# Kernel optimization log

Measured on AMD Instinct MI355X. Metric: run time of the kernel, lower is better.

Reference implementation:

```python
import jax, jax.numpy as jnp
import numpy as np

D = 1024
H = 16
FF = 4 * D


def layer_norm(x, g, b, eps=1e-5):
    mu = jnp.mean(x, axis=-1, keepdims=True)
    var = jnp.var(x, axis=-1, keepdims=True)
    return (x - mu) * jax.lax.rsqrt(var + eps) * g + b


def setup_inputs() -> dict:
    key = jax.random.key(0)
    ks = jax.random.split(key, 8)
    s = lambda fan_in: 1.0 / np.sqrt(fan_in)
    return {
        "x": jax.random.normal(ks[0], (2, 2048, D), dtype=jnp.float32),
        "ln1_g": jnp.ones((D,), jnp.float32),
        "ln1_b": jnp.zeros((D,), jnp.float32),
        "w_qkv": jax.random.uniform(ks[1], (D, 3 * D), jnp.float32, -s(D), s(D)),
        "b_qkv": jnp.zeros((3 * D,), jnp.float32),
        "w_out": jax.random.uniform(ks[2], (D, D), jnp.float32, -s(D), s(D)),
        "b_out": jnp.zeros((D,), jnp.float32),
        "ln2_g": jnp.ones((D,), jnp.float32),
        "ln2_b": jnp.zeros((D,), jnp.float32),
        "w_fc1": jax.random.uniform(ks[3], (D, FF), jnp.float32, -s(D), s(D)),
        "b_fc1": jnp.zeros((FF,), jnp.float32),
        "w_fc2": jax.random.uniform(ks[4], (FF, D), jnp.float32, -s(FF), s(FF)),
        "b_fc2": jnp.zeros((D,), jnp.float32),
    }


def reference(x, ln1_g, ln1_b, w_qkv, b_qkv, w_out, b_out,
              ln2_g, ln2_b, w_fc1, b_fc1, w_fc2, b_fc2):
    b, n, c = x.shape
    hd = c // H
    scale = hd ** -0.5

    # --- pre-norm MHA ---
    h = layer_norm(x, ln1_g, ln1_b)
    qkv = h @ w_qkv + b_qkv                      # [b,n,3c]
    qkv = qkv.reshape(b, n, 3, H, hd)
    q = jnp.transpose(qkv[:, :, 0], (0, 2, 1, 3))  # [b,H,n,hd]
    k = jnp.transpose(qkv[:, :, 1], (0, 2, 1, 3))
    v = jnp.transpose(qkv[:, :, 2], (0, 2, 1, 3))
    attn = jnp.einsum('bhqd,bhkd->bhqk', q, k) * scale
    attn = jax.nn.softmax(attn, axis=-1)
    o = jnp.einsum('bhqk,bhkd->bhqd', attn, v)   # [b,H,n,hd]
    o = jnp.transpose(o, (0, 2, 1, 3)).reshape(b, n, c)
    x = x + (o @ w_out + b_out)

    # --- pre-norm FFN ---
    h = layer_norm(x, ln2_g, ln2_b)
    h = jax.nn.gelu(h @ w_fc1 + b_fc1, approximate=False)
    x = x + (h @ w_fc2 + b_fc2)
    return x
```

## Files before the change

kernel.cpp:

```cpp
#include <hip/hip_runtime.h>
#include <stdint.h>
#include <math.h>

#define D_MODEL 1024
#define NHEAD   16
#define HDIM    64
#define FFDIM   4096
#define SEQ     2048
#define BATCH   2
#define NTOK    (BATCH*SEQ)
#define QKVN    (3*D_MODEL)

typedef __bf16 bf16;
typedef __attribute__((ext_vector_type(8))) __bf16 bf16x8;
typedef __attribute__((ext_vector_type(4))) __bf16 bf16x4;
typedef __attribute__((ext_vector_type(4))) float f32x4;

__device__ __forceinline__ void gld_lds16(const void* g, void* l) {
    __builtin_amdgcn_global_load_lds((__attribute__((address_space(1))) void*)g,
                                     (__attribute__((address_space(3))) void*)l,
                                     16, 0, 0);
}

__device__ __forceinline__ float fast_exp2(float x) {
#if __has_builtin(__builtin_amdgcn_exp2f)
    return __builtin_amdgcn_exp2f(x);
#else
    return __expf(x * 0.69314718056f);
#endif
}

__device__ __forceinline__ float fast_rcp(float x) {
#if __has_builtin(__builtin_amdgcn_rcpf)
    return __builtin_amdgcn_rcpf(x);
#else
    return 1.0f / x;
#endif
}

__device__ __forceinline__ float gelu_fast(float x) {
    float xx = x * x;
    float y  = x * fmaf(0.035677408137f, xx, 0.7978845608f);
    float z  = fminf(-2.8853900817779268f * y, 126.0f);
    float e  = fast_exp2(z);
    return x * fast_rcp(1.0f + e);
}

#define SYNC_VM(N) do {                                        \
    asm volatile("s_waitcnt vmcnt(" #N ")" ::: "memory");      \
    __builtin_amdgcn_s_barrier();                              \
    asm volatile("" ::: "memory");                             \
} while (0)

#define PHASE_BAR() do {                                       \
    asm volatile("s_waitcnt vmcnt(0)" ::: "memory");           \
    __builtin_amdgcn_s_barrier();                              \
    asm volatile("" ::: "memory");                             \
} while (0)

#define GEMM_BAR() do {                                        \
    asm volatile("s_waitcnt lgkmcnt(0)" ::: "memory");         \
    __builtin_amdgcn_s_barrier();                              \
    asm volatile("" ::: "memory");                             \
} while (0)

__global__ __launch_bounds__(256)
void k_transpose_all(const float* __restrict__ w_qkv, const float* __restrict__ w_out,
                     const float* __restrict__ w_fc1, const float* __restrict__ w_fc2,
                     bf16* __restrict__ t_qkv, bf16* __restrict__ t_out,
                     bf16* __restrict__ t_fc1, bf16* __restrict__ t_fc2) {
    __shared__ float tile[32][33];
    int bid = blockIdx.x;
    const float* W; bf16* Wt; int K, N, ti;
    if (bid < 3072)       { W = w_qkv; Wt = t_qkv; K = 1024; N = 3072; ti = bid; }
    else if (bid < 4096)  { W = w_out; Wt = t_out; K = 1024; N = 1024; ti = bid - 3072; }
    else if (bid < 8192)  { W = w_fc1; Wt = t_fc1; K = 1024; N = 4096; ti = bid - 4096; }
    else                  { W = w_fc2; Wt = t_fc2; K = 4096; N = 1024; ti = bid - 8192; }
    int tn = N >> 5;
    int n0 = (ti % tn) * 32, k0 = (ti / tn) * 32;
    int tx = threadIdx.x, ty = threadIdx.y;
#pragma unroll
    for (int i = 0; i < 4; i++)
        tile[ty + i * 8][tx] = W[(size_t)(k0 + ty + i * 8) * N + n0 + tx];
    __syncthreads();
#pragma unroll
    for (int i = 0; i < 4; i++)
        Wt[(size_t)(n0 + ty + i * 8) * K + k0 + tx] = (bf16)tile[tx][ty + i * 8];
}

__global__ __launch_bounds__(256)
void k_vtrans(const bf16* __restrict__ qkv, bf16* __restrict__ vT) {
    __shared__ bf16 t[32][33];
    int tok0 = blockIdx.x * 32, f0 = blockIdx.y * 32;
    int tx = threadIdx.x, ty = threadIdx.y;
#pragma unroll
    for (int i = 0; i < 4; i++)
        t[ty + i * 8][tx] = qkv[(size_t)(tok0 + ty + i * 8) * QKVN + 2 * D_MODEL + f0 + tx];
    __syncthreads();
    int s = tx;
    int pp = (s < 16) ? ((s >> 2) * 8 + (s & 3))
                      : (((s - 16) >> 2) * 8 + ((s - 16) & 3) + 4);
#pragma unroll
    for (int i = 0; i < 4; i++)
        vT[(size_t)(f0 + ty + i * 8) * NTOK + tok0 + pp] = t[tx][ty + i * 8];
}

__global__ __launch_bounds__(256)
void k_layernorm(const float* __restrict__ x, const float* __restrict__ g,
                 const float* __restrict__ b, bf16* __restrict__ out) {
    int row = blockIdx.x;
    int tid = threadIdx.x;
    float4 v = ((const float4*)(x + (size_t)row * D_MODEL))[tid];
    float s  = v.x + v.y + v.z + v.w;
    float ss = v.x * v.x + v.y * v.y + v.z * v.z + v.w * v.w;
#pragma unroll
    for (int off = 32; off > 0; off >>= 1) {
        s  += __shfl_down(s, off, 64);
        ss += __shfl_down(ss, off, 64);
    }
    __shared__ float red[2][4];
    __shared__ float mv[2];
    int wave = tid >> 6, lane = tid & 63;
    if (lane == 0) { red[0][wave] = s; red[1][wave] = ss; }
    __syncthreads();
    if (tid == 0) {
        float S  = red[0][0] + red[0][1] + red[0][2] + red[0][3];
        float SS = red[1][0] + red[1][1] + red[1][2] + red[1][3];
        float mu = S * (1.0f / D_MODEL);
        float var = SS * (1.0f / D_MODEL) - mu * mu;
        mv[0] = mu;
        mv[1] = rsqrtf(var + 1e-5f);
    }
    __syncthreads();
    float mu = mv[0], rs = mv[1];
    float4 gv = ((const float4*)g)[tid];
    float4 bv = ((const float4*)b)[tid];
    bf16x4 ov = { (bf16)((v.x - mu) * rs * gv.x + bv.x),
                  (bf16)((v.y - mu) * rs * gv.y + bv.y),
                  (bf16)((v.z - mu) * rs * gv.z + bv.z),
                  (bf16)((v.w - mu) * rs * gv.w + bv.w) };
    *(bf16x4*)(out + (size_t)row * D_MODEL + tid * 4) = ov;
}

template <int DO_GELU>
__global__ __launch_bounds__(512, 2)
void k_gemm256(const bf16* __restrict__ A, const bf16* __restrict__ Bt,
               const float* __restrict__ bias, bf16* __restrict__ outb,
               int M, int N, int K) {
    __shared__ bf16 LA[2][2][8192];
    __shared__ bf16 LB[2][2][8192];

    int tid = threadIdx.x;
    int wid = tid >> 6, lane = tid & 63;
    int quad = lane >> 4, l16 = lane & 15;
    int wm = (wid >> 2) * 128;
    int wn = (wid & 3) * 64;

    int nwg = gridDim.x * gridDim.y;
    int bid = blockIdx.y * gridDim.x + blockIdx.x;
    int sid = (bid & 7) * (nwg >> 3) + (bid >> 3);
    int bx = sid % gridDim.x, by = sid / gridDim.x;
    int m0 = by * 256, n0 = bx * 256;

    int l = lane;
    int rsw = l >> 2;
    int csw = 8 * ((l & 3) ^ ((l >> 3) & 3));
    const bf16* pA = A  + (size_t)(m0 + 32 * wid + rsw) * K + csw;
    const bf16* pB = Bt + (size_t)(n0 + 32 * wid + rsw) * K + csw;
    int sbase = wid * 1024;

    int xq = 8 * (quad ^ ((l16 >> 1) & 3));

    f32x4 acc[8][4];
#pragma unroll
    for (int i = 0; i < 8; i++)
#pragma unroll
        for (int j = 0; j < 4; j++) acc[i][j] = (f32x4){0.f, 0.f, 0.f, 0.f};

#define STAGE_A(buf, kh, t) do {                                               \
    gld_lds16(pA + (size_t)(t) * 64 + (kh) * 32,              &LA[buf][kh][sbase]);       \
    gld_lds16(pA + (size_t)16 * K + (size_t)(t) * 64 + (kh) * 32, &LA[buf][kh][sbase + 512]); \
} while (0)
#define STAGE_B(buf, kh, t) do {                                               \
    gld_lds16(pB + (size_t)(t) * 64 + (kh) * 32,              &LB[buf][kh][sbase]);       \
    gld_lds16(pB + (size_t)16 * K + (size_t)(t) * 64 + (kh) * 32, &LB[buf][kh][sbase + 512]); \
} while (0)

    bf16x8 af[4], bfr[4];
#define RD_B(buf, kh)  do {                                                    \
    _Pragma("unroll")                                                          \
    for (int fc = 0; fc < 4; fc++)                                             \
        bfr[fc] = *(const bf16x8*)&LB[buf][kh][(wn + fc * 16 + l16) * 32 + xq];\
} while (0)
#define RD_A(buf, kh, rh) do {                                                 \
    _Pragma("unroll")                                                          \
    for (int fr = 0; fr < 4; fr++)                                             \
        af[fr] = *(const bf16x8*)&LA[buf][kh][(wm + (rh) * 64 + fr * 16 + l16) * 32 + xq]; \
} while (0)
#define MFMA16(rh) do {                                                        \
    __builtin_amdgcn_s_setprio(1);                                             \
    _Pragma("unroll")                                                          \
    for (int fr = 0; fr < 4; fr++)                                             \
        _Pragma("unroll")                                                      \
        for (int fc = 0; fc < 4; fc++)                                         \
            acc[(rh) * 4 + fr][fc] =                                           \
                __builtin_amdgcn_mfma_f32_16x16x32_bf16(af[fr], bfr[fc],       \
                                                        acc[(rh) * 4 + fr][fc], 0, 0, 0); \
    __builtin_amdgcn_s_setprio(0);                                             \
} while (0)

    int nt = K / 64;
    int buf = 0;
    STAGE_A(0, 0, 0); STAGE_B(0, 0, 0); STAGE_A(0, 1, 0); STAGE_B(0, 1, 0);

    for (int t = 0; t < nt - 1; t++) {
        SYNC_VM(4);
        STAGE_A(buf ^ 1, 0, t + 1);
        RD_B(buf, 0); RD_A(buf, 0, 0);
        STAGE_B(buf ^ 1, 0, t + 1);
        MFMA16(0);
        RD_A(buf, 0, 1);
        MFMA16(1);
        SYNC_VM(4);
        STAGE_A(buf ^ 1, 1, t + 1);
        RD_B(buf, 1); RD_A(buf, 1, 0);
        STAGE_B(buf ^ 1, 1, t + 1);
        MFMA16(0);
        RD_A(buf, 1, 1);
        MFMA16(1);
        buf ^= 1;
    }
    SYNC_VM(4);
    RD_B(buf, 0); RD_A(buf, 0, 0);
    MFMA16(0);
    RD_A(buf, 0, 1);
    MFMA16(1);
    SYNC_VM(0);
    RD_B(buf, 1); RD_A(buf, 1, 0);
    MFMA16(0);
    RD_A(buf, 1, 1);
    MFMA16(1);

#undef STAGE_A
#undef STAGE_B
#undef RD_A
#undef RD_B
#undef MFMA16

#pragma unroll
    for (int fi = 0; fi < 8; fi++) {
        int row = m0 + wm + fi * 16 + quad * 4;
#pragma unroll
        for (int fc = 0; fc < 4; fc++) {
            int col = n0 + wn + fc * 16 + l16;
            float bb = bias[col];
#pragma unroll
            for (int r = 0; r < 4; r++) {
                float v = acc[fi][fc][r] + bb;
                if (DO_GELU) v = gelu_fast(v);
                outb[(size_t)(row + r) * N + col] = (bf16)v;
            }
        }
    }
}

template <int DO_GELU, int DO_RES, int OUT_BF16, int BN, int PIPE2, int SPLITK, int STAGE>
__global__ __launch_bounds__(256)
void k_gemm(const bf16* __restrict__ A, const bf16* __restrict__ Bt,
            const float* __restrict__ bias, const float* __restrict__ res,
            float* __restrict__ outf, bf16* __restrict__ outb,
            int M, int N, int K) {
    constexpr int WN = BN / 32;
    __shared__ bf16 As[2][128 * 32];
    __shared__ bf16 Bs[2][BN * 32];
    int tid  = threadIdx.x;
    int wave = tid >> 6, lane = tid & 63;
    int quad = lane >> 4, l16 = lane & 15;

    int nwg = gridDim.x * gridDim.y;
    int bid = blockIdx.y * gridDim.x + blockIdx.x;
    int sid = (bid & 7) * (nwg >> 3) + (bid >> 3);
    int bx = sid % gridDim.x, by = sid / gridDim.x;
    int m0 = by * 128, n0 = bx * BN;
    int wm = (wave >> 1) * 64, wn = (wave & 1) * (BN / 2);

    int Keff = (SPLITK == 2) ? (K >> 1) : K;
    int koff = (SPLITK == 2) ? blockIdx.z * Keff : 0;

    f32x4 acc[4][WN];
#pragma unroll
    for (int i = 0; i < 4; i++)
#pragma unroll
        for (int j = 0; j < WN; j++) acc[i][j] = (f32x4){0.f, 0.f, 0.f, 0.f};

    int lrow = lane >> 2;
    int lcol = (lane & 3) * 8;
    const bf16* gA0 = A + (size_t)(m0 + wave * 32 + lrow) * K + koff + lcol;
    const bf16* gA1 = gA0 + (size_t)16 * K;
    const bf16* gB0;
    const bf16* gB1 = nullptr;
    if constexpr (BN == 128) {
        gB0 = Bt + (size_t)(n0 + wave * 32 + lrow) * K + koff + lcol;
        gB1 = gB0 + (size_t)16 * K;
    } else {
        gB0 = Bt + (size_t)(n0 + wave * 16 + lrow) * K + koff + lcol;
    }

    int wA0 = wave * 1024 + lane * 8;
    int wA1 = wA0 + 512;
    int wB0 = (BN == 128) ? (wave * 1024 + lane * 8) : (wave * 512 + lane * 8);
    int wB1 = wB0 + 512;

    auto issue = [&](bf16x8* r, int k0) {
        r[0] = *(const bf16x8*)(gA0 + k0);
        r[1] = *(const bf16x8*)(gA1 + k0);
        r[2] = *(const bf16x8*)(gB0 + k0);
        if constexpr (BN == 128) r[3] = *(const bf16x8*)(gB1 + k0);
    };
    auto commit = [&](int buf, const bf16x8* r) {
        *(bf16x8*)(&As[buf][wA0]) = r[0];
        *(bf16x8*)(&As[buf][wA1]) = r[1];
        *(bf16x8*)(&Bs[buf][wB0]) = r[2];
        if constexpr (BN == 128) *(bf16x8*)(&Bs[buf][wB1]) = r[3];
    };
    auto compute = [&](const bf16* cA, const bf16* cB) {
        bf16x8 af[4], bfr[WN];
#pragma unroll
        for (int mi = 0; mi < 4; mi++)
            af[mi] = *(const bf16x8*)(cA + (wm + mi * 16 + l16) * 32 + quad * 8);
#pragma unroll
        for (int ni = 0; ni < WN; ni++)
            bfr[ni] = *(const bf16x8*)(cB + (wn + ni * 16 + l16) * 32 + quad * 8);
#pragma unroll
        for (int mi = 0; mi < 4; mi++)
#pragma unroll
            for (int ni = 0; ni < WN; ni++)
                acc[mi][ni] = __builtin_amdgcn_mfma_f32_16x16x32_bf16(af[mi], bfr[ni], acc[mi][ni], 0, 0, 0);
    };

    int niter = Keff / 32;
    if constexpr (STAGE == 1) {
        bf16* sA  = &As[0][wave * 1024];
        bf16* sB  = &Bs[0][(BN == 128) ? wave * 1024 : wave * 512];
        bf16* sA2 = &As[1][wave * 1024];
        bf16* sB2 = &Bs[1][(BN == 128) ? wave * 1024 : wave * 512];
        const bf16* rA  = &As[0][0]; const bf16* rB  = &Bs[0][0];
        const bf16* rA2 = &As[1][0]; const bf16* rB2 = &Bs[1][0];
        gld_lds16(gA0, sA);
        gld_lds16(gA1, sA + 512);
        gld_lds16(gB0, sB);
        if constexpr (BN == 128) gld_lds16(gB1, sB + 512);
        PHASE_BAR();
        for (int t = 1; t < niter; t++) {
            int k0 = t * 32;
            gld_lds16(gA0 + k0, sA2);
            gld_lds16(gA1 + k0, sA2 + 512);
            gld_lds16(gB0 + k0, sB2);
            if constexpr (BN == 128) gld_lds16(gB1 + k0, sB2 + 512);
            compute(rA, rB);
            PHASE_BAR();
            bf16* t0 = sA; sA = sA2; sA2 = t0;
            bf16* t1 = sB; sB = sB2; sB2 = t1;
            const bf16* t2 = rA; rA = rA2; rA2 = t2;
            const bf16* t3 = rB; rB = rB2; rB2 = t3;
        }
        compute(rA, rB);
    } else if constexpr (!PIPE2) {
        bf16x8 r0[4];
        issue(r0, 0);
        commit(0, r0);
        __syncthreads();
        for (int t = 1; t < niter; t++) {
            issue(r0, t * 32);
            compute(&As[(t - 1) & 1][0], &Bs[(t - 1) & 1][0]);
            commit(t & 1, r0);
            __syncthreads();
        }
        compute(&As[(niter - 1) & 1][0], &Bs[(niter - 1) & 1][0]);
    } else {
        bf16x8 r0[4], r1[4];
        issue(r0, 0);
        commit(0, r0);
        issue(r1, 32);
        GEMM_BAR();
        for (int t = 1; t + 2 < niter; t += 2) {
            issue(r0, (t + 1) * 32);
            compute(&As[0][0], &Bs[0][0]);
            commit(1, r1);
            GEMM_BAR();
            issue(r1, (t + 2) * 32);
            compute(&As[1][0], &Bs[1][0]);
            commit(0, r0);
            GEMM_BAR();
        }
        compute(&As[0][0], &Bs[0][0]);
        commit(1, r1);
        GEMM_BAR();
        compute(&As[1][0], &Bs[1][0]);
    }

#pragma unroll
    for (int mi = 0; mi < 4; mi++) {
        int row = m0 + wm + mi * 16 + quad * 4;
#pragma unroll
        for (int ni = 0; ni < WN; ni++) {
            int col = n0 + wn + ni * 16 + l16;
            if constexpr (SPLITK == 2) {
                float bb = (blockIdx.z == 0) ? bias[col] : 0.0f;
#pragma unroll
                for (int r = 0; r < 4; r++)
                    atomicAdd(&outf[(size_t)(row + r) * N + col], acc[mi][ni][r] + bb);
                continue;
            }
            float bb = bias[col];
#pragma unroll
            for (int r = 0; r < 4; r++) {
                float v = acc[mi][ni][r] + bb;
                if (DO_GELU) v = gelu_fast(v);
                size_t idx = (size_t)(row + r) * N + col;
                if (DO_RES) v += res[idx];
                if (OUT_BF16) outb[idx] = (bf16)v;
                else          outf[idx] = v;
            }
        }
    }
}

__global__ __launch_bounds__(256)
void k_attention2(const bf16* __restrict__ qkv, const bf16* __restrict__ vT,
                  bf16* __restrict__ o) {
    __shared__ bf16 Ks[2][2][64][32];
    __shared__ bf16 Vs[2][2][64][32];

    int tid = threadIdx.x, wave = tid >> 6, lane = tid & 63;
    int quad = lane >> 4, l16 = lane & 15;
    int bh = blockIdx.y;
    int b = bh >> 4, h = bh & 15;
    int q0 = blockIdx.x * 64 + wave * 16;

    const bf16* Qb  = qkv + (size_t)b * SEQ * QKVN + h * HDIM;
    const bf16* Kb  = Qb + D_MODEL;
    const bf16* vTb = vT + (size_t)h * HDIM * NTOK + b * SEQ;

    const float QSCALE = 0.125f * 1.44269504089f;
    bf16x8 qf[2];
#pragma unroll
    for (int c = 0; c < 2; c++) {
        bf16x8 qraw = *(const bf16x8*)(Qb + (size_t)(q0 + l16) * QKVN + c * 32 + quad * 8);
#pragma unroll
        for (int i = 0; i < 8; i++) qf[c][i] = (bf16)((float)qraw[i] * QSCALE);
    }

    const bf16* gK0 = Kb + (size_t)(wave * 16 + (lane >> 2)) * QKVN + (lane & 3) * 8;
    const bf16* gK1 = gK0 + 32;
    const bf16* gV0 = vTb + (size_t)(wave * 16 + (lane >> 2)) * NTOK + (lane & 3) * 8;
    const bf16* gV1 = gV0 + 32;

    f32x4 oacc[4];
#pragma unroll
    for (int i = 0; i < 4; i++) oacc[i] = (f32x4){0.f, 0.f, 0.f, 0.f};
    float lsum = 0.f;

    gld_lds16(gK0, &Ks[0][0][wave * 16][0]);
    gld_lds16(gK1, &Ks[0][1][wave * 16][0]);
    gld_lds16(gV0, &Vs[0][0][wave * 16][0]);
    gld_lds16(gV1, &Vs[0][1][wave * 16][0]);
    PHASE_BAR();

    int buf = 0;
    for (int kv0 = 0; kv0 < SEQ; kv0 += 64) {
        if (kv0 + 64 < SEQ) {
            size_t koff = (size_t)(kv0 + 64) * QKVN;
            gld_lds16(gK0 + koff, &Ks[buf ^ 1][0][wave * 16][0]);
            gld_lds16(gK1 + koff, &Ks[buf ^ 1][1][wave * 16][0]);
            gld_lds16(gV0 + kv0 + 64, &Vs[buf ^ 1][0][wave * 16][0]);
            gld_lds16(gV1 + kv0 + 64, &Vs[buf ^ 1][1][wave * 16][0]);
        }

        f32x4 s[4];
#pragma unroll
        for (int t = 0; t < 4; t++) {
            bf16x8 af0 = *(const bf16x8*)(&Ks[buf][0][t * 16 + l16][quad * 8]);
            bf16x8 af1 = *(const bf16x8*)(&Ks[buf][1][t * 16 + l16][quad * 8]);
            f32x4 z = (f32x4){0.f, 0.f, 0.f, 0.f};
            z = __builtin_amdgcn_mfma_f32_16x16x32_bf16(af0, qf[0], z, 0, 0, 0);
            z = __builtin_amdgcn_mfma_f32_16x16x32_bf16(af1, qf[1], z, 0, 0, 0);
            s[t] = z;
        }

        bf16x4 p[4];
#pragma unroll
        for (int t = 0; t < 4; t++)
#pragma unroll
            for (int r = 0; r < 4; r++) {
                float pf = fast_exp2(s[t][r]);
                lsum += pf;
                p[t][r] = (bf16)pf;
            }

#pragma unroll
        for (int tp = 0; tp < 2; tp++) {
            bf16x8 pa = __builtin_shufflevector(p[2 * tp], p[2 * tp + 1], 0, 1, 2, 3, 4, 5, 6, 7);
#pragma unroll
            for (int nt = 0; nt < 4; nt++) {
                bf16x8 vb = *(const bf16x8*)(&Vs[buf][tp][nt * 16 + l16][quad * 8]);
                oacc[nt] = __builtin_amdgcn_mfma_f32_16x16x32_bf16(pa, vb, oacc[nt], 0, 0, 0);
            }
        }

        PHASE_BAR();
        buf ^= 1;
    }

    lsum += __shfl_xor(lsum, 16, 64);
    lsum += __shfl_xor(lsum, 32, 64);
    float invl[4];
#pragma unroll
    for (int r = 0; r < 4; r++)
        invl[r] = 1.0f / __shfl(lsum, quad * 4 + r, 16);

#pragma unroll
    for (int nt = 0; nt < 4; nt++)
#pragma unroll
        for (int r = 0; r < 4; r++)
            o[(size_t)(b * SEQ + q0 + quad * 4 + r) * D_MODEL + h * HDIM + nt * 16 + l16] =
                (bf16)(oacc[nt][r] * invl[r]);
}

extern "C" void kernel_launch(void* const* d_in, const int* in_sizes, int n_in,
                              void* d_out, int out_size, void* d_ws, size_t ws_size,
                              hipStream_t stream) {
    const float* x     = (const float*)d_in[0];
    const float* ln1_g = (const float*)d_in[1];
    const float* ln1_b = (const float*)d_in[2];
    const float* w_qkv = (const float*)d_in[3];
    const float* b_qkv = (const float*)d_in[4];
    const float* w_out = (const float*)d_in[5];
    const float* b_out = (const float*)d_in[6];
    const float* ln2_g = (const float*)d_in[7];
    const float* ln2_b = (const float*)d_in[8];
    const float* w_fc1 = (const float*)d_in[9];
    const float* b_fc1 = (const float*)d_in[10];
    const float* w_fc2 = (const float*)d_in[11];
    const float* b_fc2 = (const float*)d_in[12];
    float* out = (float*)d_out;

    uintptr_t ws = (uintptr_t)d_ws;
    bf16* wt_qkv = (bf16*)(ws + 0);
    bf16* wt_out = (bf16*)(ws + 6291456);
    bf16* wt_fc1 = (bf16*)(ws + 8388608);
    bf16* wt_fc2 = (bf16*)(ws + 16777216);
    bf16* hbuf   = (bf16*)(ws + 25165824);
    bf16* vT     = hbuf;
    bf16* qkv    = (bf16*)(ws + 33554432);
    bf16* attn_o = (bf16*)(ws + 58720256);
    bf16* hgelu  = (bf16*)(ws + 33554432);

    k_transpose_all<<<12288, dim3(32, 8), 0, stream>>>(w_qkv, w_out, w_fc1, w_fc2,
                                                       wt_qkv, wt_out, wt_fc1, wt_fc2);

    k_layernorm<<<NTOK, 256, 0, stream>>>(x, ln1_g, ln1_b, hbuf);

    k_gemm256<0><<<dim3(QKVN / 256, NTOK / 256), 512, 0, stream>>>(
        hbuf, wt_qkv, b_qkv, qkv, NTOK, QKVN, D_MODEL);

    k_vtrans<<<dim3(NTOK / 32, D_MODEL / 32), dim3(32, 8), 0, stream>>>(qkv, vT);

    k_attention2<<<dim3(SEQ / 64, BATCH * NHEAD), 256, 0, stream>>>(qkv, vT, attn_o);

    k_gemm<0, 1, 0, 64, 1, 1, 0><<<dim3(D_MODEL / 64, NTOK / 128), 256, 0, stream>>>(
        attn_o, wt_out, b_out, x, out, nullptr, NTOK, D_MODEL, D_MODEL);

    k_layernorm<<<NTOK, 256, 0, stream>>>(out, ln2_g, ln2_b, hbuf);

    k_gemm256<1><<<dim3(FFDIM / 256, NTOK / 256), 512, 0, stream>>>(
        hbuf, wt_fc1, b_fc1, hgelu, NTOK, FFDIM, D_MODEL);

    k_gemm<0, 0, 0, 128, 1, 2, 0><<<dim3(D_MODEL / 128, NTOK / 128, 2), 256, 0, stream>>>(
        hgelu, wt_fc2, b_fc2, nullptr, out, nullptr, NTOK, D_MODEL, FFDIM);
}
```

Baseline: 353.3 us.

## Run FC2 on 256x256 split-K GEMM and rework k_gemm256 barrier schedule

Extends the 256x256 tile GEMM with split-K and atomic fp32 accumulation, and uses it for the FC2 projection (split into 4 along K) in place of the 128x128 split-K-by-2 kernel. It also reorders the k_gemm256 main loop so LDS reads are issued before the next global-to-LDS stage, with explicit barriers and lgkmcnt waits around each MFMA block. Unused k_gemm pipeline variants are removed. The aim is more reuse per loaded tile and better overlap in FC2, at the cost of more atomic traffic and extra barriers per k-step.

```diff
diff --git a/kernel.cpp b/kernel.cpp
--- a/kernel.cpp
+++ b/kernel.cpp
@@ -46,11 +46,12 @@
     return x * fast_rcp(1.0f + e);
 }
 
-#define SYNC_VM(N) do {                                        \
-    asm volatile("s_waitcnt vmcnt(" #N ")" ::: "memory");      \
+#define BARRIER() do {                                         \
     __builtin_amdgcn_s_barrier();                              \
     asm volatile("" ::: "memory");                             \
 } while (0)
+#define LGKM0() asm volatile("s_waitcnt lgkmcnt(0)" ::: "memory")
+#define VMW(N)  asm volatile("s_waitcnt vmcnt(" #N ")" ::: "memory")
 
 #define PHASE_BAR() do {                                       \
     asm volatile("s_waitcnt vmcnt(0)" ::: "memory");           \
@@ -142,11 +143,11 @@
     *(bf16x4*)(out + (size_t)row * D_MODEL + tid * 4) = ov;
 }
 
-template <int DO_GELU>
+template <int DO_GELU, int ATOMIC, int SPLITK>
 __global__ __launch_bounds__(512, 2)
 void k_gemm256(const bf16* __restrict__ A, const bf16* __restrict__ Bt,
                const float* __restrict__ bias, bf16* __restrict__ outb,
-               int M, int N, int K) {
+               float* __restrict__ outf, int M, int N, int K) {
     __shared__ bf16 LA[2][2][8192];
     __shared__ bf16 LB[2][2][8192];
 
@@ -162,11 +163,14 @@
     int bx = sid % gridDim.x, by = sid / gridDim.x;
     int m0 = by * 256, n0 = bx * 256;
 
+    int Keff = (SPLITK > 1) ? (K / SPLITK) : K;
+    int koff = (SPLITK > 1) ? blockIdx.z * Keff : 0;
+
     int l = lane;
     int rsw = l >> 2;
     int csw = 8 * ((l & 3) ^ ((l >> 3) & 3));
-    const bf16* pA = A  + (size_t)(m0 + 32 * wid + rsw) * K + csw;
-    const bf16* pB = Bt + (size_t)(n0 + 32 * wid + rsw) * K + csw;
+    const bf16* pA = A  + (size_t)(m0 + 32 * wid + rsw) * K + koff + csw;
+    const bf16* pB = Bt + (size_t)(n0 + 32 * wid + rsw) * K + koff + csw;
     int sbase = wid * 1024;
 
     int xq = 8 * (quad ^ ((l16 >> 1) & 3));
@@ -209,36 +213,49 @@
     __builtin_amdgcn_s_setprio(0);                                             \
 } while (0)
 
-    int nt = K / 64;
+    int nt = Keff / 64;
     int buf = 0;
-    STAGE_A(0, 0, 0); STAGE_B(0, 0, 0); STAGE_A(0, 1, 0); STAGE_B(0, 1, 0);
+    STAGE_A(0, 0, 0); STAGE_B(0, 0, 0);
+    STAGE_A(0, 1, 0); STAGE_B(0, 1, 0);
+    VMW(4); BARRIER();
 
     for (int t = 0; t < nt - 1; t++) {
-        SYNC_VM(4);
+        RD_B(buf, 0); RD_A(buf, 0, 0);
         STAGE_A(buf ^ 1, 0, t + 1);
-        RD_B(buf, 0); RD_A(buf, 0, 0);
+        BARRIER(); LGKM0();
+        MFMA16(0);
+        BARRIER();
+        RD_A(buf, 0, 1);
         STAGE_B(buf ^ 1, 0, t + 1);
+        BARRIER(); LGKM0();
+        MFMA16(1);
+        VMW(4); BARRIER();
+        RD_B(buf, 1); RD_A(buf, 1, 0);
+        STAGE_A(buf ^ 1, 1, t + 1);
+        BARRIER(); LGKM0();
         MFMA16(0);
-        RD_A(buf, 0, 1);
+        BARRIER();
+        RD_A(buf, 1, 1);
+        STAGE_B(buf ^ 1, 1, t + 1);
+        BARRIER(); LGKM0();
         MFMA16(1);
-        SYNC_VM(4);
-        STAGE_A(buf ^ 1, 1, t + 1);
-        RD_B(buf, 1); RD_A(buf, 1, 0);
-        STAGE_B(buf ^ 1, 1, t + 1);
-        MFMA16(0);
-        RD_A(buf, 1, 1);
-        MFMA16(1);
+        VMW(4); BARRIER();
         buf ^= 1;
     }
-    SYNC_VM(4);
     RD_B(buf, 0); RD_A(buf, 0, 0);
+    BARRIER(); LGKM0();
     MFMA16(0);
+    BARRIER();
     RD_A(buf, 0, 1);
+    BARRIER(); LGKM0();
     MFMA16(1);
-    SYNC_VM(0);
+    VMW(0); BARRIER();
     RD_B(buf, 1); RD_A(buf, 1, 0);
+    BARRIER(); LGKM0();
     MFMA16(0);
+    BARRIER();
     RD_A(buf, 1, 1);
+    LGKM0();
     MFMA16(1);
 
 #undef STAGE_A
@@ -253,18 +270,25 @@
 #pragma unroll
         for (int fc = 0; fc < 4; fc++) {
             int col = n0 + wn + fc * 16 + l16;
-            float bb = bias[col];
-#pragma unroll
-            for (int r = 0; r < 4; r++) {
-                float v = acc[fi][fc][r] + bb;
-                if (DO_GELU) v = gelu_fast(v);
-                outb[(size_t)(row + r) * N + col] = (bf16)v;
+            if constexpr (ATOMIC) {
+                float bb = (SPLITK == 1 || blockIdx.z == 0) ? bias[col] : 0.0f;
+#pragma unroll
+                for (int r = 0; r < 4; r++)
+                    atomicAdd(&outf[(size_t)(row + r) * N + col], acc[fi][fc][r] + bb);
+            } else {
+                float bb = bias[col];
+#pragma unroll
+                for (int r = 0; r < 4; r++) {
+                    float v = acc[fi][fc][r] + bb;
+                    if (DO_GELU) v = gelu_fast(v);
+                    outb[(size_t)(row + r) * N + col] = (bf16)v;
+                }
             }
         }
     }
 }
 
-template <int DO_GELU, int DO_RES, int OUT_BF16, int BN, int PIPE2, int SPLITK, int STAGE>
+template <int DO_GELU, int DO_RES, int OUT_BF16, int BN>
 __global__ __launch_bounds__(256)
 void k_gemm(const bf16* __restrict__ A, const bf16* __restrict__ Bt,
             const float* __restrict__ bias, const float* __restrict__ res,
@@ -284,9 +308,6 @@
     int m0 = by * 128, n0 = bx * BN;
     int wm = (wave >> 1) * 64, wn = (wave & 1) * (BN / 2);
 
-    int Keff = (SPLITK == 2) ? (K >> 1) : K;
-    int koff = (SPLITK == 2) ? blockIdx.z * Keff : 0;
-
     f32x4 acc[4][WN];
 #pragma unroll
     for (int i = 0; i < 4; i++)
@@ -295,15 +316,15 @@
 
     int lrow = lane >> 2;
     int lcol = (lane & 3) * 8;
-    const bf16* gA0 = A + (size_t)(m0 + wave * 32 + lrow) * K + koff + lcol;
+    const bf16* gA0 = A + (size_t)(m0 + wave * 32 + lrow) * K + lcol;
     const bf16* gA1 = gA0 + (size_t)16 * K;
     const bf16* gB0;
     const bf16* gB1 = nullptr;
     if constexpr (BN == 128) {
-        gB0 = Bt + (size_t)(n0 + wave * 32 + lrow) * K + koff + lcol;
+        gB0 = Bt + (size_t)(n0 + wave * 32 + lrow) * K + lcol;
         gB1 = gB0 + (size_t)16 * K;
     } else {
-        gB0 = Bt + (size_t)(n0 + wave * 16 + lrow) * K + koff + lcol;
+        gB0 = Bt + (size_t)(n0 + wave * 16 + lrow) * K + lcol;
     }
 
     int wA0 = wave * 1024 + lane * 8;
@@ -338,66 +359,26 @@
                 acc[mi][ni] = __builtin_amdgcn_mfma_f32_16x16x32_bf16(af[mi], bfr[ni], acc[mi][ni], 0, 0, 0);
     };
 
-    int niter = Keff / 32;
-    if constexpr (STAGE == 1) {
-        bf16* sA  = &As[0][wave * 1024];
-        bf16* sB  = &Bs[0][(BN == 128) ? wave * 1024 : wave * 512];
-        bf16* sA2 = &As[1][wave * 1024];
-        bf16* sB2 = &Bs[1][(BN == 128) ? wave * 1024 : wave * 512];
-        const bf16* rA  = &As[0][0]; const bf16* rB  = &Bs[0][0];
-        const bf16* rA2 = &As[1][0]; const bf16* rB2 = &Bs[1][0];
-        gld_lds16(gA0, sA);
-        gld_lds16(gA1, sA + 512);
-        gld_lds16(gB0, sB);
-        if constexpr (BN == 128) gld_lds16(gB1, sB + 512);
-        PHASE_BAR();
-        for (int t = 1; t < niter; t++) {
-            int k0 = t * 32;
-            gld_lds16(gA0 + k0, sA2);
-            gld_lds16(gA1 + k0, sA2 + 512);
-            gld_lds16(gB0 + k0, sB2);
-            if constexpr (BN == 128) gld_lds16(gB1 + k0, sB2 + 512);
-            compute(rA, rB);
-            PHASE_BAR();
-            bf16* t0 = sA; sA = sA2; sA2 = t0;
-            bf16* t1 = sB; sB = sB2; sB2 = t1;
-            const bf16* t2 = rA; rA = rA2; rA2 = t2;
-            const bf16* t3 = rB; rB = rB2; rB2 = t3;
-        }
-        compute(rA, rB);
-    } else if constexpr (!PIPE2) {
-        bf16x8 r0[4];
-        issue(r0, 0);
-        commit(0, r0);
-        __syncthreads();
-        for (int t = 1; t < niter; t++) {
-            issue(r0, t * 32);
-            compute(&As[(t - 1) & 1][0], &Bs[(t - 1) & 1][0]);
-            commit(t & 1, r0);
-            __syncthreads();
-        }
-        compute(&As[(niter - 1) & 1][0], &Bs[(niter - 1) & 1][0]);
-    } else {
-        bf16x8 r0[4], r1[4];
-        issue(r0, 0);
-        commit(0, r0);
-        issue(r1, 32);
-        GEMM_BAR();
-        for (int t = 1; t + 2 < niter; t += 2) {
-            issue(r0, (t + 1) * 32);
-            compute(&As[0][0], &Bs[0][0]);
-            commit(1, r1);
-            GEMM_BAR();
-            issue(r1, (t + 2) * 32);
-            compute(&As[1][0], &Bs[1][0]);
-            commit(0, r0);
-            GEMM_BAR();
-        }
+    int niter = K / 32;
+    bf16x8 r0[4], r1[4];
+    issue(r0, 0);
+    commit(0, r0);
+    issue(r1, 32);
+    GEMM_BAR();
+    for (int t = 1; t + 2 < niter; t += 2) {
+        issue(r0, (t + 1) * 32);
         compute(&As[0][0], &Bs[0][0]);
         commit(1, r1);
         GEMM_BAR();
+        issue(r1, (t + 2) * 32);
         compute(&As[1][0], &Bs[1][0]);
-    }
+        commit(0, r0);
+        GEMM_BAR();
+    }
+    compute(&As[0][0], &Bs[0][0]);
+    commit(1, r1);
+    GEMM_BAR();
+    compute(&As[1][0], &Bs[1][0]);
 
 #pragma unroll
     for (int mi = 0; mi < 4; mi++) {
@@ -405,13 +386,6 @@
 #pragma unroll
         for (int ni = 0; ni < WN; ni++) {
             int col = n0 + wn + ni * 16 + l16;
-            if constexpr (SPLITK == 2) {
-                float bb = (blockIdx.z == 0) ? bias[col] : 0.0f;
-#pragma unroll
-                for (int r = 0; r < 4; r++)
-                    atomicAdd(&outf[(size_t)(row + r) * N + col], acc[mi][ni][r] + bb);
-                continue;
-            }
             float bb = bias[col];
 #pragma unroll
             for (int r = 0; r < 4; r++) {
@@ -561,21 +535,21 @@
 
     k_layernorm<<<NTOK, 256, 0, stream>>>(x, ln1_g, ln1_b, hbuf);
 
-    k_gemm256<0><<<dim3(QKVN / 256, NTOK / 256), 512, 0, stream>>>(
-        hbuf, wt_qkv, b_qkv, qkv, NTOK, QKVN, D_MODEL);
+    k_gemm256<0, 0, 1><<<dim3(QKVN / 256, NTOK / 256), 512, 0, stream>>>(
+        hbuf, wt_qkv, b_qkv, qkv, nullptr, NTOK, QKVN, D_MODEL);
 
     k_vtrans<<<dim3(NTOK / 32, D_MODEL / 32), dim3(32, 8), 0, stream>>>(qkv, vT);
 
     k_attention2<<<dim3(SEQ / 64, BATCH * NHEAD), 256, 0, stream>>>(qkv, vT, attn_o);
 
-    k_gemm<0, 1, 0, 64, 1, 1, 0><<<dim3(D_MODEL / 64, NTOK / 128), 256, 0, stream>>>(
+    k_gemm<0, 1, 0, 64><<<dim3(D_MODEL / 64, NTOK / 128), 256, 0, stream>>>(
         attn_o, wt_out, b_out, x, out, nullptr, NTOK, D_MODEL, D_MODEL);
 
     k_layernorm<<<NTOK, 256, 0, stream>>>(out, ln2_g, ln2_b, hbuf);
 
-    k_gemm256<1><<<dim3(FFDIM / 256, NTOK / 256), 512, 0, stream>>>(
-        hbuf, wt_fc1, b_fc1, hgelu, NTOK, FFDIM, D_MODEL);
-
-    k_gemm<0, 0, 0, 128, 1, 2, 0><<<dim3(D_MODEL / 128, NTOK / 128, 2), 256, 0, stream>>>(
-        hgelu, wt_fc2, b_fc2, nullptr, out, nullptr, NTOK, D_MODEL, FFDIM);
-}
+    k_gemm256<1, 0, 1><<<dim3(FFDIM / 256, NTOK / 256), 512, 0, stream>>>(
+        hbuf, wt_fc1, b_fc1, hgelu, nullptr, NTOK, FFDIM, D_MODEL);
+
+    k_gemm256<0, 1, 4><<<dim3(D_MODEL / 256, NTOK / 256, 4), 512, 0, stream>>>(
+        hgelu, wt_fc2, b_fc2, nullptr, out, NTOK, D_MODEL, FFDIM);
+}
```

New measurement: 359.6 us. No clear change (+1.8%).
